# Performance work log

Hardware: AMD Instinct MI355X
Metric: run time of the kernel (lower is better)

## Reference

```python
import jax, jax.numpy as jnp
import numpy as np

TOPK_CONF = 100   # cfg.nms_top_k_conf
TOPK_IOU = 15     # cfg.nms_top_k_iou
IOU_GAUSS = (32, 32)  # cfg.iou_gauss_dim
EPS = 1e-6        # cfg.positive


def unnormal_gaussian(mask_shape, loc):
    """loc: [..., 4] = (cx, cy, w, h) in [0,1). Returns [..., H, W] unnormalized gaussians."""
    H, W = mask_shape
    ys = (jnp.arange(H, dtype=loc.dtype) + 0.5) / H  # [H]
    xs = (jnp.arange(W, dtype=loc.dtype) + 0.5) / W  # [W]
    cx, cy = loc[..., 0], loc[..., 1]
    sx = jnp.abs(loc[..., 2]) * 0.5 + 1e-3
    sy = jnp.abs(loc[..., 3]) * 0.5 + 1e-3
    dx2 = (xs - cx[..., None]) ** 2 / (2.0 * sx[..., None] ** 2)  # [..., W]
    dy2 = (ys - cy[..., None]) ** 2 / (2.0 * sy[..., None] ** 2)  # [..., H]
    return jnp.exp(-(dy2[..., :, None] + dx2[..., None, :]))      # [..., H, W]


def setup_inputs() -> dict:
    key = jax.random.key(0)
    k1, k2, k3, k4, k5 = jax.random.split(key, 5)
    B, P, C, M = 4, 19248, 81, 32
    original = jax.random.normal(k1, (B, 3, 550, 550), dtype=jnp.float32)
    loc = jax.random.uniform(k2, (B, P, 4), dtype=jnp.float32)  # cx,cy,w,h in [0,1)
    conf = jax.random.normal(k3, (B, P, C), dtype=jnp.float32)
    mask = jax.random.normal(k4, (B, P, M), dtype=jnp.float32)
    proto = jax.random.normal(k5, (B, 138, 138, M), dtype=jnp.float32)
    return {"original": original, "loc": loc, "conf": conf, "mask": mask, "proto": proto}


def reference(original, loc, conf, mask, proto):
    B, H, W = original.shape[0], original.shape[2], original.shape[3]
    # class-1 foreground confidence after softmax over classes
    conf1 = jax.nn.softmax(conf, axis=2)[:, :, 1]  # [B, P]

    # ---- detect(): top-k by conf, pairwise gaussian IoU, keep lowest-overlap boxes ----
    order = jnp.argsort(-conf1, axis=-1)[:, :TOPK_CONF]                    # [B, K]
    sconf = jnp.take_along_axis(conf1, order, axis=1)                      # [B, K]
    sloc = jnp.take_along_axis(loc, order[..., None], axis=1)              # [B, K, 4]
    smask = jnp.take_along_axis(mask, order[..., None], axis=1)            # [B, K, Mdim]

    gauss = unnormal_gaussian(IOU_GAUSS, sloc)                             # [B, K, G, G]
    g_rows = gauss[:, None, :, :, :]                                       # broadcast [B,1,K,G,G]
    g_cols = gauss[:, :, None, :, :]                                       # broadcast [B,K,1,G,G]
    inter = jnp.sum(jnp.minimum(g_rows, g_cols), axis=(-2, -1))            # [B, K, K]
    union = jnp.sum(jnp.maximum(g_rows, g_cols), axis=(-2, -1))            # [B, K, K]
    gauss_iou = inter / union
    iou_max = jnp.max(jnp.triu(gauss_iou, k=1), axis=1)                    # [B, K]
    keep = jnp.argsort(iou_max, axis=-1)[:, :TOPK_IOU]                     # [B, Kk]

    kloc = jnp.take_along_axis(sloc, keep[..., None], axis=1)              # [B, Kk, 4]
    kmask = jnp.take_along_axis(smask, keep[..., None], axis=1)            # [B, Kk, Mdim]
    kconf = jnp.take_along_axis(sconf, keep, axis=1)                       # [B, Kk]

    # ---- VarianceLoss ----
    Hp, Wp = proto.shape[1], proto.shape[2]
    ug = unnormal_gaussian((Hp, Wp), kloc)                                 # [B, Kk, Hp, Wp]
    assembled = jax.nn.sigmoid(jnp.einsum('bhwm,bkm->bkhw', proto, kmask)) # lincomb + sigmoid
    attention = assembled * ug
    mask_conf = attention * kconf[:, :, None, None]                        # einsum('abcd,ab->abcd')
    denom = jnp.sum(mask_conf, axis=1, keepdims=True) + EPS
    final_conf = 1.0 - jnp.sum(mask_conf ** 2 / denom, axis=1)             # [B, Hp, Wp]
    final_conf = jnp.where(jnp.isnan(final_conf), 0.0, final_conf)

    resized = jax.image.resize(final_conf, (B, H, W), method='bilinear')   # [B, H, W]
    total_conf = jnp.sum(resized, axis=0)                                  # [H, W]
    weighted_mean = jnp.einsum('bchw,bhw->chw', original, resized)         # [C, H, W]
    squared_diff = (original - weighted_mean) ** 2
    weighted_diff = squared_diff * resized[:, None, :, :]                  # einsum('abcd,acd->abcd')
    weighted_var = weighted_diff / (total_conf + EPS)
    return jnp.sum(weighted_var) / 100.0
```

## Files before the change

kernel.cpp:

```cpp
#include <hip/hip_runtime.h>
#include <math.h>

#define B 4
#define P 19248
#define C 81
#define M 32
#define K1 100
#define K2 15
#define G 32
#define HP 138
#define HO 550
#define FEPS 1e-6f
#define NLOC 19

#define NBUCKET 8192
#define CAP 2048

#define TI 16
#define NT 7
#define NTP 28
#define CH 128
#define NCH 8
#define SP 132

__global__ void k_conf1(const float* __restrict__ conf, float* __restrict__ conf1) {
    int gid  = blockIdx.x * blockDim.x + threadIdx.x;
    int wave = gid >> 6;
    int lane = threadIdx.x & 63;
    if (wave >= B * P) return;
    const float* row = conf + (size_t)wave * C;
    float x0 = (lane < C)      ? row[lane]      : -INFINITY;
    float x1 = (lane + 64 < C) ? row[lane + 64] : -INFINITY;
    float m = fmaxf(x0, x1);
#pragma unroll
    for (int o = 32; o; o >>= 1) m = fmaxf(m, __shfl_xor(m, o, 64));
    float s = 0.f;
    if (lane < C)      s += expf(x0 - m);
    if (lane + 64 < C) s += expf(x1 - m);
#pragma unroll
    for (int o = 32; o; o >>= 1) s += __shfl_xor(s, o, 64);
    if (lane == 0) conf1[wave] = expf(row[1] - m) / s;
}

__global__ __launch_bounds__(1024) void k_top100(
    const float* __restrict__ conf1, const float* __restrict__ loc,
    const float* __restrict__ mask,  int* __restrict__ order,
    float* __restrict__ sconf, float* __restrict__ sloc,
    float* __restrict__ smask) {
    int b = blockIdx.x;
    int tid = threadIdx.x;
    const float* c1 = conf1 + (size_t)b * P;

    __shared__ unsigned int hist[NBUCKET];
    __shared__ unsigned int gsum_[1024];
    __shared__ unsigned int g2[64];
    __shared__ unsigned long long keys[CAP];
    __shared__ int s_T;
    __shared__ int s_cnt;
    __shared__ int   s_order[K1];
    __shared__ float s_conf[K1];

    for (int i = tid; i < NBUCKET; i += 1024) hist[i] = 0;
    if (tid == 0) s_cnt = 0;
    __syncthreads();

    unsigned int mybits[NLOC];
#pragma unroll
    for (int s = 0; s < NLOC; ++s) {
        int p = tid + s * 1024;
        mybits[s] = (p < P) ? __float_as_uint(c1[p]) : 0u;
        if (p < P) atomicAdd(&hist[mybits[s] >> 17], 1u);
    }
    __syncthreads();

    {
        unsigned int gs = 0;
#pragma unroll
        for (int i = 0; i < 8; ++i) gs += hist[tid * 8 + i];
        gsum_[tid] = gs;
    }
    __syncthreads();
    if (tid < 64) {
        unsigned int gs = 0;
#pragma unroll
        for (int i = 0; i < 16; ++i) gs += gsum_[tid * 16 + i];
        g2[tid] = gs;
    }
    __syncthreads();

    if (tid == 0) {
        int cum = 0;
        int S = 63;
        for (; S > 0; --S) {
            if (cum + (int)g2[S] >= K1) break;
            cum += (int)g2[S];
        }
        int gI = S * 16 + 15;
        for (; gI > S * 16; --gI) {
            if (cum + (int)gsum_[gI] >= K1) break;
            cum += (int)gsum_[gI];
        }
        int T = gI * 8 + 7;
        for (; T > gI * 8; --T) {
            cum += (int)hist[T];
            if (cum >= K1) break;
        }
        s_T = T;
    }
    __syncthreads();

    int T = s_T;
#pragma unroll
    for (int s = 0; s < NLOC; ++s) {
        int p = tid + s * 1024;
        if (p < P && (int)(mybits[s] >> 17) >= T) {
            int pos = atomicAdd(&s_cnt, 1);
            if (pos < CAP)
                keys[pos] = ((unsigned long long)mybits[s] << 32)
                          | (unsigned int)(0xFFFFFFFFu - (unsigned int)p);
        }
    }
    __syncthreads();
    int nc = min(s_cnt, CAP);

    if (tid < nc) {
        unsigned long long mk = keys[tid];
        int rank = 0;
        for (int i = 0; i < nc; ++i) rank += (keys[i] > mk);
        if (rank < K1) {
            unsigned int bits = (unsigned int)(mk >> 32);
            int idx = (int)(0xFFFFFFFFu - (unsigned int)(mk & 0xFFFFFFFFu));
            s_order[rank] = idx;
            s_conf[rank] = __uint_as_float(bits);
        }
    }
    __syncthreads();

    for (int t = tid; t < K1; t += 1024) {
        order[b * K1 + t] = s_order[t];
        sconf[b * K1 + t] = s_conf[t];
    }
    for (int t = tid; t < K1 * 4; t += 1024) {
        int k = t >> 2, d = t & 3;
        sloc[(b * K1 + k) * 4 + d] = loc[((size_t)b * P + s_order[k]) * 4 + d];
    }
    for (int t = tid; t < K1 * M; t += 1024) {
        int k = t >> 5, d = t & 31;
        smask[(b * K1 + k) * M + d] = mask[((size_t)b * P + s_order[k]) * M + d];
    }
}

__global__ void k_gauss(const float* __restrict__ sloc, float* __restrict__ gauss) {
    int bk = blockIdx.x;
    const float* l = sloc + bk * 4;
    float cx = l[0], cy = l[1];
    float sx = fabsf(l[2]) * 0.5f + 0.001f;
    float sy = fabsf(l[3]) * 0.5f + 0.001f;
    float dsx = 2.f * sx * sx;
    float dsy = 2.f * sy * sy;
    for (int p = threadIdx.x; p < G * G; p += 256) {
        int y = p >> 5, x = p & 31;
        float xs = (x + 0.5f) / (float)G;
        float ys = (y + 0.5f) / (float)G;
        float dx2 = (xs - cx) * (xs - cx) / dsx;
        float dy2 = (ys - cy) * (ys - cy) / dsy;
        gauss[(size_t)bk * (G * G) + p] = expf(-(dy2 + dx2));
    }
}

__global__ __launch_bounds__(256) void k_iou_tile(
    const float* __restrict__ gauss, float* __restrict__ Ibuf,
    float* __restrict__ Ubuf) {
    int ch = blockIdx.x;
    int tp = blockIdx.y;
    int b  = blockIdx.z;
    int ti = 0, rem = tp;
    while (rem >= NT - ti) { rem -= NT - ti; ++ti; }
    int tj = ti + rem;

    __shared__ __align__(16) float As[TI][SP];
    __shared__ __align__(16) float Bs[TI][SP];

    int tid = threadIdx.x;
    for (int idx = tid; idx < TI * (CH / 4); idx += 256) {
        int g = idx >> 5, v = idx & 31;
        int gi = ti * TI + g;
        float4 f = make_float4(0.f, 0.f, 0.f, 0.f);
        if (gi < K1)
            f = *(const float4*)(gauss + ((size_t)(b * K1 + gi) << 10) + ch * CH + v * 4);
        *(float4*)(&As[g][v * 4]) = f;
        int gj = tj * TI + g;
        float4 h = make_float4(0.f, 0.f, 0.f, 0.f);
        if (gj < K1)
            h = *(const float4*)(gauss + ((size_t)(b * K1 + gj) << 10) + ch * CH + v * 4);
        *(float4*)(&Bs[g][v * 4]) = h;
    }
    __syncthreads();

    int li = tid >> 4, lj = tid & 15;
    int i = ti * TI + li, j = tj * TI + lj;
    if (i < j && j < K1) {
        const float4* ar = (const float4*)(&As[li][0]);
        const float4* br = (const float4*)(&Bs[lj][0]);
        float inter = 0.f, uni = 0.f;
#pragma unroll
        for (int p = 0; p < CH / 4; ++p) {
            float4 a = ar[p], c = br[p];
            inter += fminf(a.x, c.x) + fminf(a.y, c.y)
                   + fminf(a.z, c.z) + fminf(a.w, c.w);
            uni   += fmaxf(a.x, c.x) + fmaxf(a.y, c.y)
                   + fmaxf(a.z, c.z) + fmaxf(a.w, c.w);
        }
        atomicAdd(&Ibuf[(b * K1 + i) * K1 + j], inter);
        atomicAdd(&Ubuf[(b * K1 + i) * K1 + j], uni);
    }
}

__global__ void k_combine(const float* __restrict__ Ibuf, const float* __restrict__ Ubuf,
                          unsigned int* __restrict__ ioumax) {
    int gid = blockIdx.x * 256 + threadIdx.x;
    if (gid >= B * K1 * K1) return;
    int b = gid / (K1 * K1);
    int rem = gid - b * K1 * K1;
    int i = rem / K1, j = rem % K1;
    if (i >= j) return;
    float iou = Ibuf[gid] / Ubuf[gid];
    atomicMax(&ioumax[b * K1 + j], __float_as_uint(iou));
}

__global__ void k_keep(const unsigned int* __restrict__ ioumax,
                       const float* __restrict__ sloc, const float* __restrict__ smask,
                       const float* __restrict__ sconf,
                       float* __restrict__ kloc, float* __restrict__ kmask,
                       float* __restrict__ kconf) {
    int b = blockIdx.x;
    int lane = threadIdx.x;
    float v0 = (lane < K1)      ? __uint_as_float(ioumax[b * K1 + lane])      : INFINITY;
    float v1 = (lane + 64 < K1) ? __uint_as_float(ioumax[b * K1 + lane + 64]) : INFINITY;
    __shared__ int s_keep[K2];
    for (int k = 0; k < K2; ++k) {
        float bv; int bi;
        if (v0 <= v1) { bv = v0; bi = lane; }
        else          { bv = v1; bi = lane + 64; }
#pragma unroll
        for (int o = 32; o; o >>= 1) {
            float ov = __shfl_xor(bv, o, 64);
            int   oi = __shfl_xor(bi, o, 64);
            if (ov < bv || (ov == bv && oi < bi)) { bv = ov; bi = oi; }
        }
        if (bi == lane)           v0 = INFINITY;
        else if (bi == lane + 64) v1 = INFINITY;
        if (lane == 0) s_keep[k] = bi;
    }
    __syncthreads();
    for (int t = lane; t < K2 * M; t += 64) {
        int k = t >> 5, d = t & 31;
        kmask[(b * K2 + k) * M + d] = smask[(b * K1 + s_keep[k]) * M + d];
    }
    for (int t = lane; t < K2 * 4; t += 64) {
        int k = t >> 2, d = t & 3;
        kloc[(b * K2 + k) * 4 + d] = sloc[(b * K1 + s_keep[k]) * 4 + d];
    }
    if (lane < K2) kconf[b * K2 + lane] = sconf[b * K1 + s_keep[lane]];
}

__global__ __launch_bounds__(256) void k_fconf(
    const float* __restrict__ proto, const float* __restrict__ kloc,
    const float* __restrict__ kmask, const float* __restrict__ kconf,
    float* __restrict__ fconf) {
    int b = blockIdx.y;
    int px0 = blockIdx.x * 256;
    int tid = threadIdx.x;
    __shared__ float s_pv[256][M + 1];
    __shared__ float s_km[K2][M];
    __shared__ float s_loc[K2][4];
    __shared__ float s_cf[K2];
    for (int t = tid; t < K2 * M; t += 256) s_km[t >> 5][t & 31] = kmask[b * K2 * M + t];
    for (int t = tid; t < K2 * 4; t += 256) s_loc[t >> 2][t & 3] = kloc[b * K2 * 4 + t];
    if (tid < K2) s_cf[tid] = kconf[b * K2 + tid];

    int nvalid = min(256, HP * HP - px0);
    const float4* pr4 = (const float4*)(proto + ((size_t)b * (HP * HP) + px0) * M);
    for (int idx = tid; idx < nvalid * (M / 4); idx += 256) {
        float4 f = pr4[idx];
        int q = idx >> 3, v = idx & 7;
        s_pv[q][v * 4 + 0] = f.x;
        s_pv[q][v * 4 + 1] = f.y;
        s_pv[q][v * 4 + 2] = f.z;
        s_pv[q][v * 4 + 3] = f.w;
    }
    __syncthreads();

    if (tid < nvalid) {
        int p = px0 + tid;
        int h = p / HP, w = p % HP;
        float pv[M];
#pragma unroll
        for (int m = 0; m < M; ++m) pv[m] = s_pv[tid][m];
        float ys = (h + 0.5f) / (float)HP;
        float xs = (w + 0.5f) / (float)HP;
        float sum_a = 0.f, sum_a2 = 0.f;
#pragma unroll 1
        for (int k = 0; k < K2; ++k) {
            float d = 0.f;
#pragma unroll
            for (int m = 0; m < M; ++m) d += pv[m] * s_km[k][m];
            float sig = 1.f / (1.f + expf(-d));
            float cx = s_loc[k][0], cy = s_loc[k][1];
            float sx = fabsf(s_loc[k][2]) * 0.5f + 0.001f;
            float sy = fabsf(s_loc[k][3]) * 0.5f + 0.001f;
            float dx2 = (xs - cx) * (xs - cx) / (2.f * sx * sx);
            float dy2 = (ys - cy) * (ys - cy) / (2.f * sy * sy);
            float ug = expf(-(dy2 + dx2));
            float a = sig * ug * s_cf[k];
            sum_a  += a;
            sum_a2 += a * a;
        }
        float fin = 1.f - sum_a2 / (sum_a + FEPS);
        if (!(fin == fin)) fin = 0.f;
        fconf[(size_t)b * HP * HP + p] = fin;
    }
}

__global__ void k_reduce(const float* __restrict__ fconf, const float* __restrict__ original,
                         float* __restrict__ acc) {
    int idx = blockIdx.x * 256 + threadIdx.x;
    float contrib = 0.f;
    if (idx < HO * HO) {
        int y = idx / HO, x = idx % HO;
        const float scale = (float)HP / (float)HO;
        float fy = (y + 0.5f) * scale - 0.5f;
        float fx = (x + 0.5f) * scale - 0.5f;
        float y0f = floorf(fy), x0f = floorf(fx);
        float wy = fy - y0f, wx = fx - x0f;
        int y0 = (int)y0f, x0 = (int)x0f;
        int iy0 = max(y0, 0), iy1 = min(y0 + 1, HP - 1);
        int ix0 = max(x0, 0), ix1 = min(x0 + 1, HP - 1);
        float r[B];
#pragma unroll
        for (int b = 0; b < B; ++b) {
            const float* F = fconf + (size_t)b * HP * HP;
            float v00 = F[iy0 * HP + ix0], v01 = F[iy0 * HP + ix1];
            float v10 = F[iy1 * HP + ix0], v11 = F[iy1 * HP + ix1];
            r[b] = (1.f - wy) * ((1.f - wx) * v00 + wx * v01)
                 +        wy  * ((1.f - wx) * v10 + wx * v11);
        }
        float t = r[0] + r[1] + r[2] + r[3];
        float s = 0.f;
#pragma unroll
        for (int c = 0; c < 3; ++c) {
            float o[B], wm = 0.f;
#pragma unroll
            for (int b = 0; b < B; ++b) {
                o[b] = original[(((size_t)b * 3 + c) * HO + y) * HO + x];
                wm += o[b] * r[b];
            }
#pragma unroll
            for (int b = 0; b < B; ++b) {
                float d = o[b] - wm;
                s += d * d * r[b];
            }
        }
        contrib = s / (t + FEPS);
    }
    __shared__ float red[256];
    red[threadIdx.x] = contrib;
    __syncthreads();
    for (int off = 128; off; off >>= 1) {
        if (threadIdx.x < off) red[threadIdx.x] += red[threadIdx.x + off];
        __syncthreads();
    }
    if (threadIdx.x == 0) atomicAdd(acc, red[0]);
}

__global__ void k_final(const float* __restrict__ acc, float* __restrict__ out) {
    out[0] = acc[0] / 100.f;
}

extern "C" void kernel_launch(void* const* d_in, const int* in_sizes, int n_in,
                              void* d_out, int out_size, void* d_ws, size_t ws_size,
                              hipStream_t stream) {
    (void)in_sizes; (void)n_in; (void)out_size; (void)ws_size;
    const float* original = (const float*)d_in[0];
    const float* loc      = (const float*)d_in[1];
    const float* conf     = (const float*)d_in[2];
    const float* mask     = (const float*)d_in[3];
    const float* proto    = (const float*)d_in[4];

    char* ws = (char*)d_ws;
    size_t off = 0;
    auto alloc = [&](size_t bytes) -> void* {
        void* p = ws + off;
        off += (bytes + 255) & ~(size_t)255;
        return p;
    };
    float* conf1        = (float*)alloc((size_t)B * P * sizeof(float));
    int*   order        = (int*)  alloc((size_t)B * K1 * sizeof(int));
    float* sconf        = (float*)alloc((size_t)B * K1 * sizeof(float));
    float* sloc         = (float*)alloc((size_t)B * K1 * 4 * sizeof(float));
    float* smask        = (float*)alloc((size_t)B * K1 * M * sizeof(float));
    float* gauss        = (float*)alloc((size_t)B * K1 * G * G * sizeof(float));
    float* Ibuf         = (float*)alloc((size_t)B * K1 * K1 * sizeof(float));
    float* Ubuf         = (float*)alloc((size_t)B * K1 * K1 * sizeof(float));
    unsigned int* iomax = (unsigned int*)alloc((size_t)B * K1 * sizeof(unsigned int));
    float* kloc         = (float*)alloc((size_t)B * K2 * 4 * sizeof(float));
    float* kmask        = (float*)alloc((size_t)B * K2 * M * sizeof(float));
    float* kconf        = (float*)alloc((size_t)B * K2 * sizeof(float));
    float* fconf        = (float*)alloc((size_t)B * HP * HP * sizeof(float));
    float* acc          = (float*)alloc(sizeof(float));

    hipMemsetAsync(iomax, 0, (size_t)B * K1 * sizeof(unsigned int), stream);
    hipMemsetAsync(Ibuf, 0, (size_t)B * K1 * K1 * sizeof(float) * 2, stream);
    hipMemsetAsync(Ubuf, 0, (size_t)B * K1 * K1 * sizeof(float), stream);
    hipMemsetAsync(acc, 0, sizeof(float), stream);

    k_conf1<<<(B * P) / 4, 256, 0, stream>>>(conf, conf1);
    k_top100<<<B, 1024, 0, stream>>>(conf1, loc, mask, order, sconf, sloc, smask);
    k_gauss<<<B * K1, 256, 0, stream>>>(sloc, gauss);
    dim3 g4(NCH, NTP, B);
    k_iou_tile<<<g4, 256, 0, stream>>>(gauss, Ibuf, Ubuf);
    k_combine<<<(B * K1 * K1 + 255) / 256, 256, 0, stream>>>(Ibuf, Ubuf, iomax);
    k_keep<<<B, 64, 0, stream>>>(iomax, sloc, smask, sconf, kloc, kmask, kconf);
    dim3 g6((HP * HP + 255) / 256, B);
    k_fconf<<<g6, 256, 0, stream>>>(proto, kloc, kmask, kconf, fconf);
    k_reduce<<<(HO * HO + 255) / 256, 256, 0, stream>>>(fconf, original, acc);
    k_final<<<1, 1, 0, stream>>>(acc, (float*)d_out);
}
```

Measured before the change: 177.7 us.

## Fuse gaussian into top-k, merge IoU tiling with combine, fold final into reduce

Gaussian generation moves into the top-k kernel, reading the box locations from shared memory. The IoU kernel now loops over all pixel chunks inside one block, so the intersection/union buffers, their atomics and the combine kernel go away. The final divide is done by the last block of the reduction via a counter, the serial threshold scan becomes wave-level prefix sums with ballot, and the memsets are merged into one. Fewer launches and less global traffic, but the IoU grid shrinks eightfold, lowering parallelism in that stage.

```diff
diff --git a/kernel.cpp b/kernel.cpp
--- a/kernel.cpp
+++ b/kernel.cpp
@@ -42,11 +42,11 @@
     if (lane == 0) conf1[wave] = expf(row[1] - m) / s;
 }
 
-__global__ __launch_bounds__(1024) void k_top100(
+__global__ __launch_bounds__(1024) void k_top100g(
     const float* __restrict__ conf1, const float* __restrict__ loc,
-    const float* __restrict__ mask,  int* __restrict__ order,
+    const float* __restrict__ mask,
     float* __restrict__ sconf, float* __restrict__ sloc,
-    float* __restrict__ smask) {
+    float* __restrict__ smask, float* __restrict__ gauss) {
     int b = blockIdx.x;
     int tid = threadIdx.x;
     const float* c1 = conf1 + (size_t)b * P;
@@ -59,6 +59,7 @@
     __shared__ int s_cnt;
     __shared__ int   s_order[K1];
     __shared__ float s_conf[K1];
+    __shared__ float s_sloc[K1][4];
 
     for (int i = tid; i < NBUCKET; i += 1024) hist[i] = 0;
     if (tid == 0) s_cnt = 0;
@@ -88,24 +89,40 @@
     }
     __syncthreads();
 
-    if (tid == 0) {
-        int cum = 0;
-        int S = 63;
-        for (; S > 0; --S) {
-            if (cum + (int)g2[S] >= K1) break;
-            cum += (int)g2[S];
-        }
-        int gI = S * 16 + 15;
-        for (; gI > S * 16; --gI) {
-            if (cum + (int)gsum_[gI] >= K1) break;
-            cum += (int)gsum_[gI];
-        }
-        int T = gI * 8 + 7;
-        for (; T > gI * 8; --T) {
-            cum += (int)hist[T];
-            if (cum >= K1) break;
-        }
-        s_T = T;
+    if (tid < 64) {
+        unsigned int v1 = g2[tid];
+        unsigned int s1 = v1;
+#pragma unroll
+        for (int o = 1; o < 64; o <<= 1) {
+            unsigned int x = __shfl_down(s1, o, 64);
+            if (tid + o < 64) s1 += x;
+        }
+        unsigned long long m1 = __ballot((int)s1 >= K1);
+        int S = 63 - __builtin_clzll(m1);
+        int cum1 = (int)__shfl(s1, S, 64) - (int)__shfl(v1, S, 64);
+
+        unsigned int v2 = (tid < 16) ? gsum_[S * 16 + tid] : 0u;
+        unsigned int s2 = v2;
+#pragma unroll
+        for (int o = 1; o < 16; o <<= 1) {
+            unsigned int x = __shfl_down(s2, o, 64);
+            if (tid + o < 16) s2 += x;
+        }
+        unsigned long long m2 = __ballot((tid < 16) && (cum1 + (int)s2 >= K1));
+        int r2 = 63 - __builtin_clzll(m2);
+        int gI = S * 16 + r2;
+        int cum2 = cum1 + (int)__shfl(s2, r2, 64) - (int)__shfl(v2, r2, 64);
+
+        unsigned int v3 = (tid < 8) ? hist[gI * 8 + tid] : 0u;
+        unsigned int s3 = v3;
+#pragma unroll
+        for (int o = 1; o < 8; o <<= 1) {
+            unsigned int x = __shfl_down(s3, o, 64);
+            if (tid + o < 8) s3 += x;
+        }
+        unsigned long long m3 = __ballot((tid < 8) && (cum2 + (int)s3 >= K1));
+        int r3 = 63 - __builtin_clzll(m3);
+        if (tid == 0) s_T = gI * 8 + r3;
     }
     __syncthreads();
 
@@ -136,44 +153,36 @@
     }
     __syncthreads();
 
-    for (int t = tid; t < K1; t += 1024) {
-        order[b * K1 + t] = s_order[t];
-        sconf[b * K1 + t] = s_conf[t];
-    }
+    for (int t = tid; t < K1; t += 1024) sconf[b * K1 + t] = s_conf[t];
     for (int t = tid; t < K1 * 4; t += 1024) {
         int k = t >> 2, d = t & 3;
-        sloc[(b * K1 + k) * 4 + d] = loc[((size_t)b * P + s_order[k]) * 4 + d];
+        float val = loc[((size_t)b * P + s_order[k]) * 4 + d];
+        s_sloc[k][d] = val;
+        sloc[(b * K1 + k) * 4 + d] = val;
     }
     for (int t = tid; t < K1 * M; t += 1024) {
         int k = t >> 5, d = t & 31;
         smask[(b * K1 + k) * M + d] = mask[((size_t)b * P + s_order[k]) * M + d];
     }
-}
-
-__global__ void k_gauss(const float* __restrict__ sloc, float* __restrict__ gauss) {
-    int bk = blockIdx.x;
-    const float* l = sloc + bk * 4;
-    float cx = l[0], cy = l[1];
-    float sx = fabsf(l[2]) * 0.5f + 0.001f;
-    float sy = fabsf(l[3]) * 0.5f + 0.001f;
-    float dsx = 2.f * sx * sx;
-    float dsy = 2.f * sy * sy;
-    for (int p = threadIdx.x; p < G * G; p += 256) {
-        int y = p >> 5, x = p & 31;
-        float xs = (x + 0.5f) / (float)G;
-        float ys = (y + 0.5f) / (float)G;
-        float dx2 = (xs - cx) * (xs - cx) / dsx;
-        float dy2 = (ys - cy) * (ys - cy) / dsy;
-        gauss[(size_t)bk * (G * G) + p] = expf(-(dy2 + dx2));
-    }
-}
-
-__global__ __launch_bounds__(256) void k_iou_tile(
-    const float* __restrict__ gauss, float* __restrict__ Ibuf,
-    float* __restrict__ Ubuf) {
-    int ch = blockIdx.x;
-    int tp = blockIdx.y;
-    int b  = blockIdx.z;
+    __syncthreads();
+
+    int ypx = tid >> 5, xpx = tid & 31;
+    float xs = (xpx + 0.5f) / (float)G;
+    float ys = (ypx + 0.5f) / (float)G;
+    for (int k = 0; k < K1; ++k) {
+        float cx = s_sloc[k][0], cy = s_sloc[k][1];
+        float sx = fabsf(s_sloc[k][2]) * 0.5f + 0.001f;
+        float sy = fabsf(s_sloc[k][3]) * 0.5f + 0.001f;
+        float dx2 = (xs - cx) * (xs - cx) / (2.f * sx * sx);
+        float dy2 = (ys - cy) * (ys - cy) / (2.f * sy * sy);
+        gauss[((size_t)(b * K1 + k) << 10) + tid] = expf(-(dy2 + dx2));
+    }
+}
+
+__global__ __launch_bounds__(256) void k_iou(
+    const float* __restrict__ gauss, unsigned int* __restrict__ ioumax) {
+    int tp = blockIdx.x;
+    int b  = blockIdx.y;
     int ti = 0, rem = tp;
     while (rem >= NT - ti) { rem -= NT - ti; ++ti; }
     int tj = ti + rem;
@@ -182,27 +191,27 @@
     __shared__ __align__(16) float Bs[TI][SP];
 
     int tid = threadIdx.x;
-    for (int idx = tid; idx < TI * (CH / 4); idx += 256) {
-        int g = idx >> 5, v = idx & 31;
-        int gi = ti * TI + g;
-        float4 f = make_float4(0.f, 0.f, 0.f, 0.f);
-        if (gi < K1)
-            f = *(const float4*)(gauss + ((size_t)(b * K1 + gi) << 10) + ch * CH + v * 4);
-        *(float4*)(&As[g][v * 4]) = f;
-        int gj = tj * TI + g;
-        float4 h = make_float4(0.f, 0.f, 0.f, 0.f);
-        if (gj < K1)
-            h = *(const float4*)(gauss + ((size_t)(b * K1 + gj) << 10) + ch * CH + v * 4);
-        *(float4*)(&Bs[g][v * 4]) = h;
-    }
-    __syncthreads();
-
     int li = tid >> 4, lj = tid & 15;
     int i = ti * TI + li, j = tj * TI + lj;
-    if (i < j && j < K1) {
+    float inter = 0.f, uni = 0.f;
+
+    for (int ch = 0; ch < NCH; ++ch) {
+        for (int idx = tid; idx < TI * (CH / 4); idx += 256) {
+            int g = idx >> 5, v = idx & 31;
+            int gi = ti * TI + g;
+            float4 f = make_float4(0.f, 0.f, 0.f, 0.f);
+            if (gi < K1)
+                f = *(const float4*)(gauss + ((size_t)(b * K1 + gi) << 10) + ch * CH + v * 4);
+            *(float4*)(&As[g][v * 4]) = f;
+            int gj = tj * TI + g;
+            float4 h = make_float4(0.f, 0.f, 0.f, 0.f);
+            if (gj < K1)
+                h = *(const float4*)(gauss + ((size_t)(b * K1 + gj) << 10) + ch * CH + v * 4);
+            *(float4*)(&Bs[g][v * 4]) = h;
+        }
+        __syncthreads();
         const float4* ar = (const float4*)(&As[li][0]);
         const float4* br = (const float4*)(&Bs[lj][0]);
-        float inter = 0.f, uni = 0.f;
 #pragma unroll
         for (int p = 0; p < CH / 4; ++p) {
             float4 a = ar[p], c = br[p];
@@ -211,21 +220,10 @@
             uni   += fmaxf(a.x, c.x) + fmaxf(a.y, c.y)
                    + fmaxf(a.z, c.z) + fmaxf(a.w, c.w);
         }
-        atomicAdd(&Ibuf[(b * K1 + i) * K1 + j], inter);
-        atomicAdd(&Ubuf[(b * K1 + i) * K1 + j], uni);
-    }
-}
-
-__global__ void k_combine(const float* __restrict__ Ibuf, const float* __restrict__ Ubuf,
-                          unsigned int* __restrict__ ioumax) {
-    int gid = blockIdx.x * 256 + threadIdx.x;
-    if (gid >= B * K1 * K1) return;
-    int b = gid / (K1 * K1);
-    int rem = gid - b * K1 * K1;
-    int i = rem / K1, j = rem % K1;
-    if (i >= j) return;
-    float iou = Ibuf[gid] / Ubuf[gid];
-    atomicMax(&ioumax[b * K1 + j], __float_as_uint(iou));
+        __syncthreads();
+    }
+    if (i < j && j < K1)
+        atomicMax(&ioumax[b * K1 + j], __float_as_uint(inter / uni));
 }
 
 __global__ void k_keep(const unsigned int* __restrict__ ioumax,
@@ -323,7 +321,8 @@
 }
 
 __global__ void k_reduce(const float* __restrict__ fconf, const float* __restrict__ original,
-                         float* __restrict__ acc) {
+                         float* __restrict__ acc, unsigned int* __restrict__ count,
+                         float* __restrict__ out) {
     int idx = blockIdx.x * 256 + threadIdx.x;
     float contrib = 0.f;
     if (idx < HO * HO) {
@@ -370,11 +369,16 @@
         if (threadIdx.x < off) red[threadIdx.x] += red[threadIdx.x + off];
         __syncthreads();
     }
-    if (threadIdx.x == 0) atomicAdd(acc, red[0]);
-}
-
-__global__ void k_final(const float* __restrict__ acc, float* __restrict__ out) {
-    out[0] = acc[0] / 100.f;
+    if (threadIdx.x == 0) {
+        atomicAdd(acc, red[0]);
+        __threadfence();
+        unsigned int prev = atomicAdd(count, 1u);
+        if (prev == gridDim.x - 1) {
+            __threadfence();
+            float total = atomicAdd(acc, 0.0f);
+            out[0] = total / 100.f;
+        }
+    }
 }
 
 extern "C" void kernel_launch(void* const* d_in, const int* in_sizes, int n_in,
@@ -395,34 +399,27 @@
         return p;
     };
     float* conf1        = (float*)alloc((size_t)B * P * sizeof(float));
-    int*   order        = (int*)  alloc((size_t)B * K1 * sizeof(int));
     float* sconf        = (float*)alloc((size_t)B * K1 * sizeof(float));
     float* sloc         = (float*)alloc((size_t)B * K1 * 4 * sizeof(float));
     float* smask        = (float*)alloc((size_t)B * K1 * M * sizeof(float));
     float* gauss        = (float*)alloc((size_t)B * K1 * G * G * sizeof(float));
-    float* Ibuf         = (float*)alloc((size_t)B * K1 * K1 * sizeof(float));
-    float* Ubuf         = (float*)alloc((size_t)B * K1 * K1 * sizeof(float));
-    unsigned int* iomax = (unsigned int*)alloc((size_t)B * K1 * sizeof(unsigned int));
     float* kloc         = (float*)alloc((size_t)B * K2 * 4 * sizeof(float));
     float* kmask        = (float*)alloc((size_t)B * K2 * M * sizeof(float));
     float* kconf        = (float*)alloc((size_t)B * K2 * sizeof(float));
     float* fconf        = (float*)alloc((size_t)B * HP * HP * sizeof(float));
-    float* acc          = (float*)alloc(sizeof(float));
-
-    hipMemsetAsync(iomax, 0, (size_t)B * K1 * sizeof(unsigned int), stream);
-    hipMemsetAsync(Ibuf, 0, (size_t)B * K1 * K1 * sizeof(float) * 2, stream);
-    hipMemsetAsync(Ubuf, 0, (size_t)B * K1 * K1 * sizeof(float), stream);
-    hipMemsetAsync(acc, 0, sizeof(float), stream);
+    unsigned int* iomax = (unsigned int*)alloc((size_t)B * K1 * sizeof(unsigned int));
+    float*        acc   = (float*)alloc(sizeof(float));
+    unsigned int* count = (unsigned int*)alloc(sizeof(unsigned int));
+
+    hipMemsetAsync(iomax, 0, 1792 + 256 + 256, stream);
 
     k_conf1<<<(B * P) / 4, 256, 0, stream>>>(conf, conf1);
-    k_top100<<<B, 1024, 0, stream>>>(conf1, loc, mask, order, sconf, sloc, smask);
-    k_gauss<<<B * K1, 256, 0, stream>>>(sloc, gauss);
-    dim3 g4(NCH, NTP, B);
-    k_iou_tile<<<g4, 256, 0, stream>>>(gauss, Ibuf, Ubuf);
-    k_combine<<<(B * K1 * K1 + 255) / 256, 256, 0, stream>>>(Ibuf, Ubuf, iomax);
+    k_top100g<<<B, 1024, 0, stream>>>(conf1, loc, mask, sconf, sloc, smask, gauss);
+    dim3 g4(NTP, B);
+    k_iou<<<g4, 256, 0, stream>>>(gauss, iomax);
     k_keep<<<B, 64, 0, stream>>>(iomax, sloc, smask, sconf, kloc, kmask, kconf);
     dim3 g6((HP * HP + 255) / 256, B);
     k_fconf<<<g6, 256, 0, stream>>>(proto, kloc, kmask, kconf, fconf);
-    k_reduce<<<(HO * HO + 255) / 256, 256, 0, stream>>>(fconf, original, acc);
-    k_final<<<1, 1, 0, stream>>>(acc, (float*)d_out);
-}
+    k_reduce<<<(HO * HO + 255) / 256, 256, 0, stream>>>(fconf, original, acc, count,
+                                                        (float*)d_out);
+}
```

Measured after the change: 236.5 us. +33.0%, slower.

## Split top-k selection into parallel histogram, threshold, compact and finish kernels

Applied to the files above, without the earlier changes.

The histogram is now built with global atomics inside the softmax kernel. The single-block-per-batch top-100 kernel is split into a threshold kernel (wave-scan search), a grid-wide compaction kernel and a small ranking kernel. The final divide is folded into the reduce kernel through a last-block counter, and the multiple memsets are merged into one contiguous memset. This targets the serial 4-block top-k stage and per-launch overhead, at the cost of global atomic contention on the histogram and extra kernel launches.

```diff
diff --git a/kernel.cpp b/kernel.cpp
--- a/kernel.cpp
+++ b/kernel.cpp
@@ -11,7 +11,6 @@
 #define HP 138
 #define HO 550
 #define FEPS 1e-6f
-#define NLOC 19
 
 #define NBUCKET 8192
 #define CAP 2048
@@ -23,7 +22,8 @@
 #define NCH 8
 #define SP 132
 
-__global__ void k_conf1(const float* __restrict__ conf, float* __restrict__ conf1) {
+__global__ void k_conf1(const float* __restrict__ conf, float* __restrict__ conf1,
+                        unsigned int* __restrict__ ghist) {
     int gid  = blockIdx.x * blockDim.x + threadIdx.x;
     int wave = gid >> 6;
     int lane = threadIdx.x & 63;
@@ -39,112 +39,120 @@
     if (lane + 64 < C) s += expf(x1 - m);
 #pragma unroll
     for (int o = 32; o; o >>= 1) s += __shfl_xor(s, o, 64);
-    if (lane == 0) conf1[wave] = expf(row[1] - m) / s;
-}
-
-__global__ __launch_bounds__(1024) void k_top100(
-    const float* __restrict__ conf1, const float* __restrict__ loc,
-    const float* __restrict__ mask,  int* __restrict__ order,
-    float* __restrict__ sconf, float* __restrict__ sloc,
-    float* __restrict__ smask) {
+    if (lane == 0) {
+        float v = expf(row[1] - m) / s;
+        conf1[wave] = v;
+        int b = wave / P;
+        atomicAdd(&ghist[b * NBUCKET + (__float_as_uint(v) >> 17)], 1u);
+    }
+}
+
+__global__ __launch_bounds__(1024) void k_thresh(
+    const unsigned int* __restrict__ ghist, int* __restrict__ Tout) {
     int b = blockIdx.x;
     int tid = threadIdx.x;
-    const float* c1 = conf1 + (size_t)b * P;
-
     __shared__ unsigned int hist[NBUCKET];
     __shared__ unsigned int gsum_[1024];
     __shared__ unsigned int g2[64];
-    __shared__ unsigned long long keys[CAP];
-    __shared__ int s_T;
-    __shared__ int s_cnt;
+    for (int i = tid; i < NBUCKET; i += 1024) hist[i] = ghist[b * NBUCKET + i];
+    __syncthreads();
+    {
+        unsigned int gs = 0;
+#pragma unroll
+        for (int i = 0; i < 8; ++i) gs += hist[tid * 8 + i];
+        gsum_[tid] = gs;
+    }
+    __syncthreads();
+    if (tid < 64) {
+        unsigned int gs = 0;
+#pragma unroll
+        for (int i = 0; i < 16; ++i) gs += gsum_[tid * 16 + i];
+        g2[tid] = gs;
+    }
+    __syncthreads();
+    if (tid < 64) {
+        unsigned int v1 = g2[tid];
+        unsigned int s1 = v1;
+#pragma unroll
+        for (int o = 1; o < 64; o <<= 1) {
+            unsigned int x = __shfl_down(s1, o, 64);
+            if (tid + o < 64) s1 += x;
+        }
+        unsigned long long m1 = __ballot((int)s1 >= K1);
+        int S = 63 - __builtin_clzll(m1);
+        int cum1 = (int)__shfl(s1, S, 64) - (int)__shfl(v1, S, 64);
+
+        unsigned int v2 = (tid < 16) ? gsum_[S * 16 + tid] : 0u;
+        unsigned int s2 = v2;
+#pragma unroll
+        for (int o = 1; o < 16; o <<= 1) {
+            unsigned int x = __shfl_down(s2, o, 64);
+            if (tid + o < 16) s2 += x;
+        }
+        unsigned long long m2 = __ballot((tid < 16) && (cum1 + (int)s2 >= K1));
+        int r2 = 63 - __builtin_clzll(m2);
+        int gI = S * 16 + r2;
+        int cum2 = cum1 + (int)__shfl(s2, r2, 64) - (int)__shfl(v2, r2, 64);
+
+        unsigned int v3 = (tid < 8) ? hist[gI * 8 + tid] : 0u;
+        unsigned int s3 = v3;
+#pragma unroll
+        for (int o = 1; o < 8; o <<= 1) {
+            unsigned int x = __shfl_down(s3, o, 64);
+            if (tid + o < 8) s3 += x;
+        }
+        unsigned long long m3 = __ballot((tid < 8) && (cum2 + (int)s3 >= K1));
+        int r3 = 63 - __builtin_clzll(m3);
+        if (tid == 0) Tout[b] = gI * 8 + r3;
+    }
+}
+
+__global__ __launch_bounds__(1024) void k_compact(
+    const float* __restrict__ conf1, const int* __restrict__ Tin,
+    unsigned int* __restrict__ cnt, unsigned long long* __restrict__ cand) {
+    int b = blockIdx.y;
+    int p = blockIdx.x * 1024 + threadIdx.x;
+    if (p >= P) return;
+    unsigned int bits = __float_as_uint(conf1[(size_t)b * P + p]);
+    if ((int)(bits >> 17) >= Tin[b]) {
+        unsigned int pos = atomicAdd(&cnt[b], 1u);
+        if (pos < CAP)
+            cand[b * CAP + pos] = ((unsigned long long)bits << 32)
+                                | (unsigned int)(0xFFFFFFFFu - (unsigned int)p);
+    }
+}
+
+__global__ __launch_bounds__(256) void k_finish(
+    const unsigned int* __restrict__ cnt, const unsigned long long* __restrict__ cand,
+    const float* __restrict__ loc, const float* __restrict__ mask,
+    float* __restrict__ sconf, float* __restrict__ sloc, float* __restrict__ smask) {
+    int b = blockIdx.x;
+    int tid = threadIdx.x;
+    __shared__ unsigned long long s_keys[CAP];
     __shared__ int   s_order[K1];
     __shared__ float s_conf[K1];
-
-    for (int i = tid; i < NBUCKET; i += 1024) hist[i] = 0;
-    if (tid == 0) s_cnt = 0;
-    __syncthreads();
-
-    unsigned int mybits[NLOC];
-#pragma unroll
-    for (int s = 0; s < NLOC; ++s) {
-        int p = tid + s * 1024;
-        mybits[s] = (p < P) ? __float_as_uint(c1[p]) : 0u;
-        if (p < P) atomicAdd(&hist[mybits[s] >> 17], 1u);
-    }
-    __syncthreads();
-
-    {
-        unsigned int gs = 0;
-#pragma unroll
-        for (int i = 0; i < 8; ++i) gs += hist[tid * 8 + i];
-        gsum_[tid] = gs;
-    }
-    __syncthreads();
-    if (tid < 64) {
-        unsigned int gs = 0;
-#pragma unroll
-        for (int i = 0; i < 16; ++i) gs += gsum_[tid * 16 + i];
-        g2[tid] = gs;
-    }
-    __syncthreads();
-
-    if (tid == 0) {
-        int cum = 0;
-        int S = 63;
-        for (; S > 0; --S) {
-            if (cum + (int)g2[S] >= K1) break;
-            cum += (int)g2[S];
-        }
-        int gI = S * 16 + 15;
-        for (; gI > S * 16; --gI) {
-            if (cum + (int)gsum_[gI] >= K1) break;
-            cum += (int)gsum_[gI];
-        }
-        int T = gI * 8 + 7;
-        for (; T > gI * 8; --T) {
-            cum += (int)hist[T];
-            if (cum >= K1) break;
-        }
-        s_T = T;
-    }
-    __syncthreads();
-
-    int T = s_T;
-#pragma unroll
-    for (int s = 0; s < NLOC; ++s) {
-        int p = tid + s * 1024;
-        if (p < P && (int)(mybits[s] >> 17) >= T) {
-            int pos = atomicAdd(&s_cnt, 1);
-            if (pos < CAP)
-                keys[pos] = ((unsigned long long)mybits[s] << 32)
-                          | (unsigned int)(0xFFFFFFFFu - (unsigned int)p);
-        }
-    }
-    __syncthreads();
-    int nc = min(s_cnt, CAP);
-
-    if (tid < nc) {
-        unsigned long long mk = keys[tid];
+    int nc = min((int)cnt[b], CAP);
+    int ncp = (nc + 7) & ~7;
+    for (int t = tid; t < ncp; t += 256)
+        s_keys[t] = (t < nc) ? cand[b * CAP + t] : 0ULL;
+    __syncthreads();
+    for (int t = tid; t < nc; t += 256) {
+        unsigned long long mk = s_keys[t];
         int rank = 0;
-        for (int i = 0; i < nc; ++i) rank += (keys[i] > mk);
+#pragma unroll 8
+        for (int i = 0; i < ncp; ++i) rank += (s_keys[i] > mk);
         if (rank < K1) {
-            unsigned int bits = (unsigned int)(mk >> 32);
-            int idx = (int)(0xFFFFFFFFu - (unsigned int)(mk & 0xFFFFFFFFu));
-            s_order[rank] = idx;
-            s_conf[rank] = __uint_as_float(bits);
-        }
-    }
-    __syncthreads();
-
-    for (int t = tid; t < K1; t += 1024) {
-        order[b * K1 + t] = s_order[t];
-        sconf[b * K1 + t] = s_conf[t];
-    }
-    for (int t = tid; t < K1 * 4; t += 1024) {
+            s_order[rank] = (int)(0xFFFFFFFFu - (unsigned int)(mk & 0xFFFFFFFFu));
+            s_conf[rank] = __uint_as_float((unsigned int)(mk >> 32));
+        }
+    }
+    __syncthreads();
+    for (int t = tid; t < K1; t += 256) sconf[b * K1 + t] = s_conf[t];
+    for (int t = tid; t < K1 * 4; t += 256) {
         int k = t >> 2, d = t & 3;
         sloc[(b * K1 + k) * 4 + d] = loc[((size_t)b * P + s_order[k]) * 4 + d];
     }
-    for (int t = tid; t < K1 * M; t += 1024) {
+    for (int t = tid; t < K1 * M; t += 256) {
         int k = t >> 5, d = t & 31;
         smask[(b * K1 + k) * M + d] = mask[((size_t)b * P + s_order[k]) * M + d];
     }
@@ -323,7 +331,8 @@
 }
 
 __global__ void k_reduce(const float* __restrict__ fconf, const float* __restrict__ original,
-                         float* __restrict__ acc) {
+                         float* __restrict__ acc, unsigned int* __restrict__ count,
+                         float* __restrict__ out) {
     int idx = blockIdx.x * 256 + threadIdx.x;
     float contrib = 0.f;
     if (idx < HO * HO) {
@@ -370,11 +379,16 @@
         if (threadIdx.x < off) red[threadIdx.x] += red[threadIdx.x + off];
         __syncthreads();
     }
-    if (threadIdx.x == 0) atomicAdd(acc, red[0]);
-}
-
-__global__ void k_final(const float* __restrict__ acc, float* __restrict__ out) {
-    out[0] = acc[0] / 100.f;
+    if (threadIdx.x == 0) {
+        atomicAdd(acc, red[0]);
+        __threadfence();
+        unsigned int prev = atomicAdd(count, 1u);
+        if (prev == gridDim.x - 1) {
+            __threadfence();
+            float total = atomicAdd(acc, 0.0f);
+            out[0] = total / 100.f;
+        }
+    }
 }
 
 extern "C" void kernel_launch(void* const* d_in, const int* in_sizes, int n_in,
@@ -394,28 +408,33 @@
         off += (bytes + 255) & ~(size_t)255;
         return p;
     };
+    unsigned int* ghist = (unsigned int*)alloc((size_t)B * NBUCKET * sizeof(unsigned int));
+    float* Ibuf         = (float*)alloc((size_t)B * K1 * K1 * sizeof(float));
+    float* Ubuf         = (float*)alloc((size_t)B * K1 * K1 * sizeof(float));
+    unsigned int* cnt   = (unsigned int*)alloc((size_t)B * sizeof(unsigned int));
+    unsigned int* iomax = (unsigned int*)alloc((size_t)B * K1 * sizeof(unsigned int));
+    float*        acc   = (float*)alloc(sizeof(float));
+    unsigned int* count = (unsigned int*)alloc(sizeof(unsigned int));
+    size_t zero_bytes = off;
     float* conf1        = (float*)alloc((size_t)B * P * sizeof(float));
-    int*   order        = (int*)  alloc((size_t)B * K1 * sizeof(int));
+    int*   Tbuf         = (int*)  alloc((size_t)B * sizeof(int));
+    unsigned long long* cand = (unsigned long long*)alloc((size_t)B * CAP * sizeof(unsigned long long));
     float* sconf        = (float*)alloc((size_t)B * K1 * sizeof(float));
     float* sloc         = (float*)alloc((size_t)B * K1 * 4 * sizeof(float));
     float* smask        = (float*)alloc((size_t)B * K1 * M * sizeof(float));
     float* gauss        = (float*)alloc((size_t)B * K1 * G * G * sizeof(float));
-    float* Ibuf         = (float*)alloc((size_t)B * K1 * K1 * sizeof(float));
-    float* Ubuf         = (float*)alloc((size_t)B * K1 * K1 * sizeof(float));
-    unsigned int* iomax = (unsigned int*)alloc((size_t)B * K1 * sizeof(unsigned int));
     float* kloc         = (float*)alloc((size_t)B * K2 * 4 * sizeof(float));
     float* kmask        = (float*)alloc((size_t)B * K2 * M * sizeof(float));
     float* kconf        = (float*)alloc((size_t)B * K2 * sizeof(float));
     float* fconf        = (float*)alloc((size_t)B * HP * HP * sizeof(float));
-    float* acc          = (float*)alloc(sizeof(float));
-
-    hipMemsetAsync(iomax, 0, (size_t)B * K1 * sizeof(unsigned int), stream);
-    hipMemsetAsync(Ibuf, 0, (size_t)B * K1 * K1 * sizeof(float) * 2, stream);
-    hipMemsetAsync(Ubuf, 0, (size_t)B * K1 * K1 * sizeof(float), stream);
-    hipMemsetAsync(acc, 0, sizeof(float), stream);
-
-    k_conf1<<<(B * P) / 4, 256, 0, stream>>>(conf, conf1);
-    k_top100<<<B, 1024, 0, stream>>>(conf1, loc, mask, order, sconf, sloc, smask);
+
+    hipMemsetAsync(ws, 0, zero_bytes, stream);
+
+    k_conf1<<<(B * P) / 4, 256, 0, stream>>>(conf, conf1, ghist);
+    k_thresh<<<B, 1024, 0, stream>>>(ghist, Tbuf);
+    dim3 gc((P + 1023) / 1024, B);
+    k_compact<<<gc, 1024, 0, stream>>>(conf1, Tbuf, cnt, cand);
+    k_finish<<<B, 256, 0, stream>>>(cnt, cand, loc, mask, sconf, sloc, smask);
     k_gauss<<<B * K1, 256, 0, stream>>>(sloc, gauss);
     dim3 g4(NCH, NTP, B);
     k_iou_tile<<<g4, 256, 0, stream>>>(gauss, Ibuf, Ubuf);
@@ -423,6 +442,6 @@
     k_keep<<<B, 64, 0, stream>>>(iomax, sloc, smask, sconf, kloc, kmask, kconf);
     dim3 g6((HP * HP + 255) / 256, B);
     k_fconf<<<g6, 256, 0, stream>>>(proto, kloc, kmask, kconf, fconf);
-    k_reduce<<<(HO * HO + 255) / 256, 256, 0, stream>>>(fconf, original, acc);
-    k_final<<<1, 1, 0, stream>>>(acc, (float*)d_out);
-}
+    k_reduce<<<(HO * HO + 255) / 256, 256, 0, stream>>>(fconf, original, acc, count,
+                                                        (float*)d_out);
+}
```

After: 249.1 us. +40.2%, slower.
